# Performance work log

Measured on AMD Instinct MI355X. Metric: run time of the kernel, lower is better.

## Reference

```python
import jax, jax.numpy as jnp
import numpy as np


def setup_inputs() -> dict:
    key = jax.random.key(0)
    ks = jax.random.split(key, 10)
    B, S, H, I, V = 64, 2048, 512, 512, 50257
    scale = 0.05
    return {
        "last_output": jax.random.randint(ks[0], (B,), 0, V),
        "last_hidden": jax.random.normal(ks[1], (1, B, H), jnp.float32),
        "encoder_outputs": jax.random.normal(ks[2], (S, B, H), jnp.float32),
        "embedding": jax.random.normal(ks[3], (V, I), jnp.float32) * scale,
        "W_ih": jax.random.normal(ks[4], (3 * H, I + H), jnp.float32) * scale,
        "b_ih": jax.random.normal(ks[5], (3 * H,), jnp.float32) * scale,
        "W_hh": jax.random.normal(ks[6], (3 * H, H), jnp.float32) * scale,
        "b_hh": jax.random.normal(ks[7], (3 * H,), jnp.float32) * scale,
        "W_out": jax.random.normal(ks[8], (V, 2 * H), jnp.float32) * scale,
        "b_out": jax.random.normal(ks[9], (V,), jnp.float32) * scale,
    }


def _gru_step(x, h, W_ih, b_ih, W_hh, b_hh):
    # torch nn.GRU parametrization, single layer, single timestep.
    H = h.shape[-1]
    gi = x @ W_ih.T + b_ih  # [B, 3H]
    gh = h @ W_hh.T + b_hh  # [B, 3H]
    i_r, i_z, i_n = gi[:, :H], gi[:, H:2 * H], gi[:, 2 * H:]
    h_r, h_z, h_n = gh[:, :H], gh[:, H:2 * H], gh[:, 2 * H:]
    r = jax.nn.sigmoid(i_r + h_r)
    z = jax.nn.sigmoid(i_z + h_z)
    n = jnp.tanh(i_n + r * h_n)
    return (1.0 - z) * n + z * h


def reference(last_output, last_hidden, encoder_outputs, embedding,
              W_ih, b_ih, W_hh, b_hh, W_out, b_out):
    # Embedding lookup: [B, I]
    embedded = embedding[last_output]
    h_top = last_hidden[-1]  # [B, H]
    # Luong 'dot' attention: score(b, s) = h_b . enc[s, b]
    scores = jnp.einsum('bh,sbh->bs', h_top, encoder_outputs)  # [B, S]
    attn = jax.nn.softmax(scores, axis=-1)                      # [B, S]
    # context = attn @ enc (per batch): [B, H]
    context = jnp.einsum('bs,sbh->bh', attn, encoder_outputs)
    # GRU single step on cat(embedded, context)
    rnn_in = jnp.concatenate([embedded, context], axis=-1)      # [B, I+H]
    h_new = _gru_step(rnn_in, h_top, W_ih, b_ih, W_hh, b_hh)    # [B, H]
    # Output projection on cat(rnn_out, context) -> log_softmax over vocab
    feat = jnp.concatenate([h_new, context], axis=-1)           # [B, 2H]
    logits = feat @ W_out.T + b_out                             # [B, V]
    logp = jax.nn.log_softmax(logits, axis=-1)
    hidden = h_new[None]  # [1, B, H]
    return logp, hidden
```

## Files before the change

kernel.cpp:

```cpp
#include <hip/hip_runtime.h>
#include <hip/hip_bf16.h>
#include <math.h>

#define BB 64
#define SS 2048
#define HH 512
#define VV 50257
#define KD 1024
#define NSPLIT 32
#define NTILE 786

typedef float f32x4 __attribute__((ext_vector_type(4)));
typedef __bf16 bf16x8 __attribute__((ext_vector_type(8)));
typedef __attribute__((address_space(3))) void lds_void;
typedef __attribute__((address_space(1))) const void glb_void;

__device__ __forceinline__ float dot4(float4 a, float4 b) {
  return a.x*b.x + a.y*b.y + a.z*b.z + a.w*b.w;
}

__device__ __forceinline__ bf16x8 cvt8(float4 a, float4 b) {
  bf16x8 r;
  r[0]=(__bf16)a.x; r[1]=(__bf16)a.y; r[2]=(__bf16)a.z; r[3]=(__bf16)a.w;
  r[4]=(__bf16)b.x; r[5]=(__bf16)b.y; r[6]=(__bf16)b.z; r[7]=(__bf16)b.w;
  return r;
}

__device__ __forceinline__ size_t fragAddr(int b, int k) {
  return (size_t)(k >> 5)*2048 + (size_t)(b >> 4)*512
       + (size_t)((k >> 3) & 3)*128 + (size_t)(b & 15)*8 + (size_t)(k & 7);
}

__global__ __launch_bounds__(256) void attn_partial(
    const float* __restrict__ hprev, const float* __restrict__ enc,
    float* __restrict__ pm, float* __restrict__ pl, float* __restrict__ pacc)
{
  const int b = blockIdx.x >> 5;
  const int split = blockIdx.x & 31;
  const int t = threadIdx.x;
  const int w = t >> 6, lane = t & 63;

  const float* hb = hprev + b*HH + lane*8;
  const float4 h0 = *(const float4*)hb;
  const float4 h1 = *(const float4*)(hb + 4);
  const int s0 = split*64 + w*16;

  float m = -INFINITY, lsum = 0.f;
  float acc[8];
#pragma unroll
  for (int j = 0; j < 8; ++j) acc[j] = 0.f;

#pragma unroll 1
  for (int half = 0; half < 2; ++half) {
    float4 ea[8], eb[8];
#pragma unroll
    for (int i = 0; i < 8; ++i) {
      const float* ep = enc + ((size_t)(s0 + half*8 + i)*BB + b)*HH + lane*8;
      ea[i] = *(const float4*)ep; eb[i] = *(const float4*)(ep + 4);
    }
    float dd[8];
#pragma unroll
    for (int i = 0; i < 8; ++i) dd[i] = dot4(h0, ea[i]) + dot4(h1, eb[i]);
#pragma unroll
    for (int off = 32; off >= 1; off >>= 1) {
#pragma unroll
      for (int i = 0; i < 8; ++i) dd[i] += __shfl_xor(dd[i], off, 64);
    }
    float hm = dd[0];
#pragma unroll
    for (int i = 1; i < 8; ++i) hm = fmaxf(hm, dd[i]);
    const float mn = fmaxf(m, hm);
    const float sc = __expf(m - mn);
    float p[8], psum = 0.f;
#pragma unroll
    for (int i = 0; i < 8; ++i) { p[i] = __expf(dd[i] - mn); psum += p[i]; }
    lsum = lsum*sc + psum;
#pragma unroll
    for (int j = 0; j < 8; ++j) acc[j] *= sc;
#pragma unroll
    for (int i = 0; i < 8; ++i) {
      acc[0] += p[i]*ea[i].x; acc[1] += p[i]*ea[i].y;
      acc[2] += p[i]*ea[i].z; acc[3] += p[i]*ea[i].w;
      acc[4] += p[i]*eb[i].x; acc[5] += p[i]*eb[i].y;
      acc[6] += p[i]*eb[i].z; acc[7] += p[i]*eb[i].w;
    }
    m = mn;
  }

  __shared__ float sm4[4], sl4[4];
  __shared__ float sacc[4][HH];
  if (lane == 0) { sm4[w] = m; sl4[w] = lsum; }
  __syncthreads();
  const float M = fmaxf(fmaxf(sm4[0], sm4[1]), fmaxf(sm4[2], sm4[3]));
  const float ew = __expf(m - M);
#pragma unroll
  for (int j = 0; j < 8; ++j) sacc[w][lane*8 + j] = acc[j]*ew;
  __syncthreads();

  const int rec = blockIdx.x;
  for (int hh = t; hh < HH; hh += 256)
    pacc[(size_t)rec*HH + hh] = sacc[0][hh]+sacc[1][hh]+sacc[2][hh]+sacc[3][hh];
  if (t == 0) {
    float L = sl4[0]*__expf(sm4[0]-M) + sl4[1]*__expf(sm4[1]-M)
            + sl4[2]*__expf(sm4[2]-M) + sl4[3]*__expf(sm4[3]-M);
    pm[rec] = M; pl[rec] = L;
  }
}

__global__ __launch_bounds__(256) void attn_reduce(
    const float* __restrict__ pm, const float* __restrict__ pl,
    const float* __restrict__ pacc, __hip_bfloat16* __restrict__ featA)
{
  const int b = blockIdx.x, t = threadIdx.x;
  __shared__ float smm[NSPLIT], sll[NSPLIT], sco[NSPLIT];
  if (t < NSPLIT) { smm[t] = pm[b*NSPLIT + t]; sll[t] = pl[b*NSPLIT + t]; }
  __syncthreads();
  float M = -INFINITY;
  for (int q = 0; q < NSPLIT; ++q) M = fmaxf(M, smm[q]);
  float L = 0.f;
  for (int q = 0; q < NSPLIT; ++q) L += sll[q]*__expf(smm[q]-M);
  const float inv = 1.f/L;
  if (t < NSPLIT) sco[t] = __expf(smm[t]-M)*inv;
  __syncthreads();
  const int hh0 = 2*t;
  float s0 = 0.f, s1 = 0.f;
  for (int q = 0; q < NSPLIT; ++q) {
    const float* pq = pacc + ((size_t)b*NSPLIT + q)*HH;
    s0 += pq[hh0]   * sco[q];
    s1 += pq[hh0+1] * sco[q];
  }
  const size_t a = fragAddr(b, HH + hh0);
  featA[a]   = (__hip_bfloat16)s0;
  featA[a+1] = (__hip_bfloat16)s1;
}

__global__ __launch_bounds__(256) void gru_gemm(
    const int* __restrict__ last_out, const float* __restrict__ emb,
    const float* __restrict__ hprev, const __hip_bfloat16* __restrict__ featA,
    const float* __restrict__ W_ih, const float* __restrict__ W_hh,
    float* __restrict__ gates)
{
  const int u = blockIdx.x;
  const int gt = u / 12;
  const int rem = u % 12;
  const int seg = rem >> 2, ks = rem & 3;
  const int w = threadIdx.x >> 6, lane = threadIdx.x & 63;
  const int col = lane & 15, kg = lane >> 4;
  const int g = gt*64 + w*16 + col;

  const float* wrow = (seg == 2) ? (W_hh + (size_t)g*HH)
                                 : (W_ih + (size_t)g*KD + seg*HH);
  int lo_r[4];
#pragma unroll
  for (int mt = 0; mt < 4; ++mt) lo_r[mt] = last_out[mt*16 + col];

  f32x4 acc[4];
#pragma unroll
  for (int mt = 0; mt < 4; ++mt) acc[mt] = (f32x4){0.f,0.f,0.f,0.f};

  const int kbeg = ks*128, kend = kbeg + 128;
  for (int k0 = kbeg; k0 < kend; k0 += 32) {
    const float* wp = wrow + k0 + kg*8;
    const bf16x8 bf = cvt8(*(const float4*)wp, *(const float4*)(wp+4));
#pragma unroll
    for (int mt = 0; mt < 4; ++mt) {
      const int bb = mt*16 + col;
      bf16x8 af;
      if (seg == 0) {
        const float* ap = emb + (size_t)lo_r[mt]*HH + k0 + kg*8;
        af = cvt8(*(const float4*)ap, *(const float4*)(ap+4));
      } else if (seg == 1) {
        af = *(const bf16x8*)(featA + fragAddr(bb, HH + k0 + kg*8));
      } else {
        const float* ap = hprev + (size_t)bb*HH + k0 + kg*8;
        af = cvt8(*(const float4*)ap, *(const float4*)(ap+4));
      }
      acc[mt] = __builtin_amdgcn_mfma_f32_16x16x32_bf16(af, bf, acc[mt], 0, 0, 0);
    }
  }

  float* gp = gates + (size_t)rem*BB*1536;
#pragma unroll
  for (int mt = 0; mt < 4; ++mt)
#pragma unroll
    for (int reg = 0; reg < 4; ++reg) {
      const int brow = mt*16 + kg*4 + reg;
      gp[(size_t)brow*1536 + g] = acc[mt][reg];
    }
}

__global__ __launch_bounds__(512) void gru_pointwise(
    const float* __restrict__ gates, const float* __restrict__ hprev,
    const float* __restrict__ b_ih, const float* __restrict__ b_hh,
    float* __restrict__ hid_out, __hip_bfloat16* __restrict__ featA)
{
  const int b = blockIdx.x, j = threadIdx.x;

  float i_r = 0.f, i_z = 0.f, i_n = 0.f;
#pragma unroll
  for (int p = 0; p < 8; ++p) {
    const float* gp = gates + ((size_t)p*BB + b)*1536;
    i_r += gp[j]; i_z += gp[HH + j]; i_n += gp[2*HH + j];
  }
  float h_r = 0.f, h_z = 0.f, h_n = 0.f;
#pragma unroll
  for (int p = 8; p < 12; ++p) {
    const float* gp = gates + ((size_t)p*BB + b)*1536;
    h_r += gp[j]; h_z += gp[HH + j]; h_n += gp[2*HH + j];
  }

  const float r = 1.f/(1.f + __expf(-(i_r + h_r + b_ih[j] + b_hh[j])));
  const float z = 1.f/(1.f + __expf(-(i_z + h_z + b_ih[HH+j] + b_hh[HH+j])));
  const float n = tanhf(i_n + b_ih[2*HH+j] + r*(h_n + b_hh[2*HH+j]));
  const float hp = hprev[b*HH + j];
  const float hn = (1.f - z)*n + z*hp;
  hid_out[b*HH + j] = hn;
  featA[fragAddr(b, j)] = (__hip_bfloat16)hn;
}

__global__ __launch_bounds__(256) void logits_gemm(
    const __hip_bfloat16* __restrict__ featA, const float* __restrict__ W_out,
    const float* __restrict__ b_out, float* __restrict__ out,
    float* __restrict__ pmE, float* __restrict__ plE)
{
  __shared__ float smem[8192];
  __shared__ float pMq[4*64], pLq[4*64];
  const int tile = blockIdx.x;
  const int t = threadIdx.x;
  const int w = t >> 6, lane = t & 63;
  const int col = lane & 15, kg = lane >> 4;
  const int vbase = tile*64;
  const int v = vbase + w*16 + col;

  const __hip_bfloat16* fp = featA + lane*8;
  const int rowL = w*16 + col;
  const int sXor = (rowL & 7) << 2;

  auto stage = [&](int buf, int kc) {
#pragma unroll
    for (int i = 0; i < 4; ++i) {
      const int sigma = (w*4 + i)*64 + lane;
      const int row = sigma >> 4;
      const int t16 = sigma & 15;
      const int kdl = (t16*4) ^ ((row & 7) << 2);
      int grow = vbase + row; if (grow > VV-1) grow = VV-1;
      const float* src = W_out + (size_t)grow*KD + kc*64 + kdl;
      __builtin_amdgcn_global_load_lds((glb_void*)src,
          (lds_void*)(smem + buf*4096 + (w*4 + i)*256), 16, 0, 0);
    }
  };

  f32x4 acc[4];
#pragma unroll
  for (int mt = 0; mt < 4; ++mt) acc[mt] = (f32x4){0.f,0.f,0.f,0.f};

  int buf = 0;
  stage(0, 0);
  __syncthreads();

#pragma unroll 1
  for (int kc = 0; kc < 16; ++kc) {
    if (kc + 1 < 16) stage(buf ^ 1, kc + 1);
    const float* wt = smem + buf*4096;
#pragma unroll
    for (int h = 0; h < 2; ++h) {
      const int kin = h*32 + kg*8;
      const float4 wa = *(const float4*)(wt + rowL*64 + (kin ^ sXor));
      const float4 wb = *(const float4*)(wt + rowL*64 + ((kin + 4) ^ sXor));
      const bf16x8 bf = cvt8(wa, wb);
      const __hip_bfloat16* f = fp + (size_t)(kc*2 + h)*2048;
      acc[0] = __builtin_amdgcn_mfma_f32_16x16x32_bf16(*(const bf16x8*)(f),        bf, acc[0], 0, 0, 0);
      acc[1] = __builtin_amdgcn_mfma_f32_16x16x32_bf16(*(const bf16x8*)(f + 512),  bf, acc[1], 0, 0, 0);
      acc[2] = __builtin_amdgcn_mfma_f32_16x16x32_bf16(*(const bf16x8*)(f + 1024), bf, acc[2], 0, 0, 0);
      acc[3] = __builtin_amdgcn_mfma_f32_16x16x32_bf16(*(const bf16x8*)(f + 1536), bf, acc[3], 0, 0, 0);
    }
    __syncthreads();
    buf ^= 1;
  }

  float* vals = smem;
  const float bo = (v < VV) ? b_out[v] : 0.f;
#pragma unroll
  for (int mt = 0; mt < 4; ++mt)
#pragma unroll
    for (int reg = 0; reg < 4; ++reg) {
      const float val = acc[mt][reg] + bo;
      const int brow = mt*16 + kg*4 + reg;
      if (v < VV) out[(size_t)brow*VV + v] = val;
      vals[brow*65 + w*16 + col] = (v < VV) ? val : -INFINITY;
    }
  __syncthreads();

  {
    const int row = t & 63, q = t >> 6;
    const float* vr = vals + row*65 + q*16;
    float M = -INFINITY;
#pragma unroll
    for (int i = 0; i < 16; ++i) M = fmaxf(M, vr[i]);
    float L = 0.f;
    if (M > -INFINITY) {
#pragma unroll
      for (int i = 0; i < 16; ++i) L += __expf(vr[i] - M);
    }
    pMq[q*64 + row] = M; pLq[q*64 + row] = L;
  }
  __syncthreads();
  if (t < 64) {
    float M = pMq[t], L = pLq[t];
#pragma unroll
    for (int q = 1; q < 4; ++q) {
      const float mq = pMq[q*64 + t], lq = pLq[q*64 + t];
      if (mq > -INFINITY) {
        const float mn = fmaxf(M, mq);
        L = L*__expf(M - mn) + lq*__expf(mq - mn);
        M = mn;
      }
    }
    pmE[t*1024 + tile] = M; plE[t*1024 + tile] = L;
  }
}

__global__ __launch_bounds__(256) void lsm_sub(
    float* __restrict__ out, const float* __restrict__ pmE,
    const float* __restrict__ plE)
{
  const int t = threadIdx.x;
  const int wv = t >> 6, lane = t & 63;
  const size_t off = (size_t)blockIdx.x * 1024;
  const size_t total = (size_t)BB*VV;
  __shared__ float cs[2];
  __shared__ int rowA_s;

  if (wv < 2) {
    size_t pos = (wv == 0) ? off : (off + 1023 < total ? off + 1023 : total - 1);
    const int row = (int)(pos / VV);
    float M = -INFINITY, L = 0.f;
    for (int q = lane; q < NTILE; q += 64) {
      const float mq = pmE[row*1024 + q], lq = plE[row*1024 + q];
      const float mn = fmaxf(M, mq);
      L = L*__expf(M - mn) + lq*__expf(mq - mn);
      M = mn;
    }
#pragma unroll
    for (int o = 32; o >= 1; o >>= 1) {
      const float m2 = __shfl_xor(M, o, 64), l2 = __shfl_xor(L, o, 64);
      const float mn = fmaxf(M, m2);
      L = L*__expf(M - mn) + l2*__expf(m2 - mn);
      M = mn;
    }
    if (lane == 0) {
      cs[wv] = M + logf(L);
      if (wv == 0) rowA_s = row;
    }
  }
  __syncthreads();

  const size_t i = off + (size_t)t*4;
  if (i >= total) return;
  const size_t rs = (size_t)(rowA_s + 1)*VV;
  float4 v = *(float4*)(out + i);
  v.x -= (i     >= rs) ? cs[1] : cs[0];
  v.y -= (i + 1 >= rs) ? cs[1] : cs[0];
  v.z -= (i + 2 >= rs) ? cs[1] : cs[0];
  v.w -= (i + 3 >= rs) ? cs[1] : cs[0];
  *(float4*)(out + i) = v;
}

extern "C" void kernel_launch(void* const* d_in, const int* in_sizes, int n_in,
                              void* d_out, int out_size, void* d_ws, size_t ws_size,
                              hipStream_t stream)
{
  const int*   last_output = (const int*)d_in[0];
  const float* last_hidden = (const float*)d_in[1];
  const float* enc         = (const float*)d_in[2];
  const float* emb         = (const float*)d_in[3];
  const float* W_ih        = (const float*)d_in[4];
  const float* b_ih        = (const float*)d_in[5];
  const float* W_hh        = (const float*)d_in[6];
  const float* b_hh        = (const float*)d_in[7];
  const float* W_out       = (const float*)d_in[8];
  const float* b_out       = (const float*)d_in[9];
  float* out = (float*)d_out;

  __hip_bfloat16* featA = (__hip_bfloat16*)d_ws;
  float* gates = (float*)((char*)d_ws + 131072);
  float* pm   = gates + (size_t)12*BB*1536;
  float* pl   = pm + BB*NSPLIT;
  float* pmE  = pl + BB*NSPLIT;
  float* plE  = pmE + BB*1024;
  float* pacc = out;
  float* hid_out = out + (size_t)BB*VV;

  attn_partial <<<dim3(BB*NSPLIT), dim3(256), 0, stream>>>(last_hidden, enc, pm, pl, pacc);
  attn_reduce  <<<dim3(BB),        dim3(256), 0, stream>>>(pm, pl, pacc, featA);
  gru_gemm     <<<dim3(24*12),     dim3(256), 0, stream>>>(last_output, emb, last_hidden,
                                                           featA, W_ih, W_hh, gates);
  gru_pointwise<<<dim3(BB),        dim3(512), 0, stream>>>(gates, last_hidden, b_ih, b_hh,
                                                           hid_out, featA);
  logits_gemm  <<<dim3(NTILE),     dim3(256), 0, stream>>>(featA, W_out, b_out, out, pmE, plE);
  lsm_sub      <<<dim3((int)(((size_t)BB*VV + 1023)/1024)), dim3(256), 0, stream>>>(out, pmE, plE);
}
```

Baseline: 157.7 us.

## Split logits GEMM along K into two halves with separate combine kernel

The logits GEMM is split along the reduction dimension into two blocks per vocab tile, doubling the block count to improve occupancy across CUs. Each block writes fp32 partial results to workspace, and a new combine kernel sums the halves, adds the bias, writes the logits and computes the per-tile max/sum-exp. Double buffering is removed in favour of single-buffer staging with a launch-bounds occupancy hint. This adds an extra kernel launch and a partial-buffer write and read of roughly 25 MB round trip.

```diff
diff --git a/kernel.cpp b/kernel.cpp
--- a/kernel.cpp
+++ b/kernel.cpp
@@ -218,25 +218,23 @@
   featA[fragAddr(b, j)] = (__hip_bfloat16)hn;
 }
 
-__global__ __launch_bounds__(256) void logits_gemm(
+__global__ __launch_bounds__(256, 4) void gemm_ks(
     const __hip_bfloat16* __restrict__ featA, const float* __restrict__ W_out,
-    const float* __restrict__ b_out, float* __restrict__ out,
-    float* __restrict__ pmE, float* __restrict__ plE)
-{
-  __shared__ float smem[8192];
-  __shared__ float pMq[4*64], pLq[4*64];
-  const int tile = blockIdx.x;
+    float* __restrict__ partial)
+{
+  __shared__ float wtile[4096];
+  const int bid = blockIdx.x;
+  const int tile = bid >> 1, half = bid & 1;
   const int t = threadIdx.x;
   const int w = t >> 6, lane = t & 63;
   const int col = lane & 15, kg = lane >> 4;
   const int vbase = tile*64;
-  const int v = vbase + w*16 + col;
-
-  const __hip_bfloat16* fp = featA + lane*8;
   const int rowL = w*16 + col;
   const int sXor = (rowL & 7) << 2;
 
-  auto stage = [&](int buf, int kc) {
+  const __hip_bfloat16* fp = featA + (size_t)half*16*2048 + lane*8;
+
+  auto stage = [&](int kc) {
 #pragma unroll
     for (int i = 0; i < 4; ++i) {
       const int sigma = (w*4 + i)*64 + lane;
@@ -244,9 +242,9 @@
       const int t16 = sigma & 15;
       const int kdl = (t16*4) ^ ((row & 7) << 2);
       int grow = vbase + row; if (grow > VV-1) grow = VV-1;
-      const float* src = W_out + (size_t)grow*KD + kc*64 + kdl;
+      const float* src = W_out + (size_t)grow*KD + half*512 + kc*64 + kdl;
       __builtin_amdgcn_global_load_lds((glb_void*)src,
-          (lds_void*)(smem + buf*4096 + (w*4 + i)*256), 16, 0, 0);
+          (lds_void*)(wtile + (w*4 + i)*256), 16, 0, 0);
     }
   };
 
@@ -254,19 +252,15 @@
 #pragma unroll
   for (int mt = 0; mt < 4; ++mt) acc[mt] = (f32x4){0.f,0.f,0.f,0.f};
 
-  int buf = 0;
-  stage(0, 0);
-  __syncthreads();
-
 #pragma unroll 1
-  for (int kc = 0; kc < 16; ++kc) {
-    if (kc + 1 < 16) stage(buf ^ 1, kc + 1);
-    const float* wt = smem + buf*4096;
+  for (int kc = 0; kc < 8; ++kc) {
+    stage(kc);
+    __syncthreads();
 #pragma unroll
     for (int h = 0; h < 2; ++h) {
       const int kin = h*32 + kg*8;
-      const float4 wa = *(const float4*)(wt + rowL*64 + (kin ^ sXor));
-      const float4 wb = *(const float4*)(wt + rowL*64 + ((kin + 4) ^ sXor));
+      const float4 wa = *(const float4*)(wtile + rowL*64 + (kin ^ sXor));
+      const float4 wb = *(const float4*)(wtile + rowL*64 + ((kin + 4) ^ sXor));
       const bf16x8 bf = cvt8(wa, wb);
       const __hip_bfloat16* f = fp + (size_t)(kc*2 + h)*2048;
       acc[0] = __builtin_amdgcn_mfma_f32_16x16x32_bf16(*(const bf16x8*)(f),        bf, acc[0], 0, 0, 0);
@@ -275,20 +269,49 @@
       acc[3] = __builtin_amdgcn_mfma_f32_16x16x32_bf16(*(const bf16x8*)(f + 1536), bf, acc[3], 0, 0, 0);
     }
     __syncthreads();
-    buf ^= 1;
-  }
-
-  float* vals = smem;
-  const float bo = (v < VV) ? b_out[v] : 0.f;
+  }
+
+  float* pout = partial + (size_t)bid*4096;
 #pragma unroll
   for (int mt = 0; mt < 4; ++mt)
 #pragma unroll
     for (int reg = 0; reg < 4; ++reg) {
-      const float val = acc[mt][reg] + bo;
       const int brow = mt*16 + kg*4 + reg;
-      if (v < VV) out[(size_t)brow*VV + v] = val;
-      vals[brow*65 + w*16 + col] = (v < VV) ? val : -INFINITY;
-    }
+      pout[brow*64 + w*16 + col] = acc[mt][reg];
+    }
+}
+
+__global__ __launch_bounds__(256) void combine(
+    const float* __restrict__ partial, const float* __restrict__ b_out,
+    float* __restrict__ out, float* __restrict__ pmE, float* __restrict__ plE)
+{
+  __shared__ float vals[64*65];
+  __shared__ float pMq[4*64], pLq[4*64];
+  const int tile = blockIdx.x;
+  const int t = threadIdx.x;
+  const int vbase = tile*64;
+  const float* p0 = partial + (size_t)(tile*2 + 0)*4096;
+  const float* p1 = partial + (size_t)(tile*2 + 1)*4096;
+
+#pragma unroll
+  for (int j = 0; j < 4; ++j) {
+    const int i = t*16 + j*4;
+    const float4 f0 = *(const float4*)(p0 + i);
+    const float4 f1 = *(const float4*)(p1 + i);
+    const int brow = i >> 6, vcol = i & 63;
+#pragma unroll
+    for (int e = 0; e < 4; ++e) {
+      const int v = vbase + vcol + e;
+      const float pe = (e==0 ? f0.x+f1.x : e==1 ? f0.y+f1.y : e==2 ? f0.z+f1.z : f0.w+f1.w);
+      if (v < VV) {
+        const float val = pe + b_out[v];
+        out[(size_t)brow*VV + v] = val;
+        vals[brow*65 + vcol + e] = val;
+      } else {
+        vals[brow*65 + vcol + e] = -INFINITY;
+      }
+    }
+  }
   __syncthreads();
 
   {
@@ -384,10 +407,11 @@
 
   __hip_bfloat16* featA = (__hip_bfloat16*)d_ws;
   float* gates = (float*)((char*)d_ws + 131072);
-  float* pm   = gates + (size_t)12*BB*1536;
-  float* pl   = pm + BB*NSPLIT;
-  float* pmE  = pl + BB*NSPLIT;
-  float* plE  = pmE + BB*1024;
+  float* pm    = gates + (size_t)12*BB*1536;
+  float* pl    = pm + BB*NSPLIT;
+  float* pmE   = pl + BB*NSPLIT;
+  float* plE   = pmE + BB*1024;
+  float* partial = plE + BB*1024;
   float* pacc = out;
   float* hid_out = out + (size_t)BB*VV;
 
@@ -397,6 +421,7 @@
                                                            featA, W_ih, W_hh, gates);
   gru_pointwise<<<dim3(BB),        dim3(512), 0, stream>>>(gates, last_hidden, b_ih, b_hh,
                                                            hid_out, featA);
-  logits_gemm  <<<dim3(NTILE),     dim3(256), 0, stream>>>(featA, W_out, b_out, out, pmE, plE);
+  gemm_ks      <<<dim3(NTILE*2),   dim3(256), 0, stream>>>(featA, W_out, partial);
+  combine      <<<dim3(NTILE),     dim3(256), 0, stream>>>(partial, b_out, out, pmE, plE);
   lsm_sub      <<<dim3((int)(((size_t)BB*VV + 1023)/1024)), dim3(256), 0, stream>>>(out, pmE, plE);
 }
```

New measurement: 187.2 us. +18.7%, slower.
